# Kernel optimization log

Measured on AMD Instinct MI355X. Metric: run time of the kernel, lower is better.

## Reference

```python
import jax, jax.numpy as jnp
import numpy as np

T, B, DIM, N = 2048, 8, 1024, 64

def setup_inputs() -> dict:
    key = jax.random.key(0)
    ks = jax.random.split(key, 6)
    scale = 1.0 / np.sqrt(DIM)  # xavier-ish for Linear(dim, n_state)
    return {
        "x": jax.random.normal(ks[0], (T, B, DIM), dtype=jnp.float32),
        "S0": jnp.zeros((B, N, N), dtype=jnp.float32),
        "W_k": jax.random.normal(ks[1], (N, DIM), dtype=jnp.float32) * scale,
        "W_v": jax.random.normal(ks[2], (N, DIM), dtype=jnp.float32) * scale,
        "W_q": jax.random.normal(ks[3], (N, DIM), dtype=jnp.float32) * scale,
        "W_alpha": jax.random.normal(ks[4], (N, DIM), dtype=jnp.float32) * scale,
        "b_alpha": jnp.full((N,), 2.0, dtype=jnp.float32),
        "d_g": jnp.full((N,), 0.5, dtype=jnp.float32),
        "b_g": jnp.zeros((N,), dtype=jnp.float32),
    }

def reference(x, S0, W_k, W_v, W_q, W_alpha, b_alpha, d_g, b_g):
    # Precompute all projections: [T, B, N]
    k_all = jnp.einsum('tbd,nd->tbn', x, W_k)
    v_all = jnp.einsum('tbd,nd->tbn', x, W_v)
    q_all = jnp.einsum('tbd,nd->tbn', x, W_q)
    alpha_all = jax.nn.sigmoid(jnp.einsum('tbd,nd->tbn', x, W_alpha) + b_alpha)

    def step(S, inp):
        k, v, q, alpha = inp  # each [B, N]
        retrieved = jnp.einsum('bij,bj->bi', S, k)          # S @ k
        g = jax.nn.sigmoid(d_g * retrieved + b_g)
        v_gated = v * g
        outer_vk = jnp.einsum('bi,bj->bij', v_gated, k)
        S = alpha[..., None] * S + (1.0 - alpha[..., None]) * outer_vk
        out = jnp.einsum('bij,bj->bi', S, q)                # S @ q
        out = out * jax.nn.silu(out)                        # self-gate
        return S, out

    S_final, output = jax.lax.scan(step, S0, (k_all, v_all, q_all, alpha_all))
    return output, S_final
```

## Files before the change

kernel.cpp:

```cpp
#include <hip/hip_runtime.h>

#define TT 2048
#define BB 8
#define DD 1024
#define NN 64
#define C64 64
#define NC2 (TT / C64)

typedef __attribute__((ext_vector_type(8))) short bfrag;
typedef __attribute__((ext_vector_type(4))) float f32x4;
typedef __attribute__((ext_vector_type(8))) unsigned short ushort8;

__device__ __forceinline__ float rcp_(float x) { return __builtin_amdgcn_rcpf(x); }
__device__ __forceinline__ float exp2_(float x) {
#if __has_builtin(__builtin_amdgcn_exp2f)
    return __builtin_amdgcn_exp2f(x);
#else
    return exp2f(x);
#endif
}
__device__ __forceinline__ float sigmoidf_(float x) {
    return rcp_(1.0f + __expf(-x));
}
__device__ __forceinline__ float bcastlane(float x, int l) {
    return __int_as_float(__builtin_amdgcn_readlane(__float_as_int(x), l));
}

__device__ __forceinline__ unsigned short cvt_bf16(float f) {
    unsigned int u = __float_as_uint(f);
    return (unsigned short)((u + 0x7FFF + ((u >> 16) & 1)) >> 16);
}

__device__ __forceinline__ void gll16(const float* g, float* l) {
    __builtin_amdgcn_global_load_lds(
        (const __attribute__((address_space(1))) void*)g,
        (__attribute__((address_space(3))) void*)l, 16, 0, 0);
}

__global__ __launch_bounds__(256) void proj_gemm_kernel(
    const float* __restrict__ x,
    const float* __restrict__ W0, const float* __restrict__ W1,
    const float* __restrict__ W2, const float* __restrict__ W3,
    const float* __restrict__ b_alpha,
    float* __restrict__ O0, float* __restrict__ O1,
    float* __restrict__ O2, float* __restrict__ O3)
{
    const int mat = blockIdx.x;
    const float* __restrict__ W = (mat == 0) ? W0 : (mat == 1) ? W1 : (mat == 2) ? W2 : W3;
    float* __restrict__ C       = (mat == 0) ? O0 : (mat == 1) ? O1 : (mat == 2) ? O2 : O3;

    const int m0   = blockIdx.y * 128;
    const int tid  = threadIdx.x;
    const int lane = tid & 63;
    const int wave = tid >> 6;
    const int ln   = lane & 15;
    const int q8   = (lane >> 4) * 8;

    __shared__ unsigned short As[128][40];
    __shared__ unsigned short Bs[64][40];

    f32x4 acc[2][4] = {};

    const int arow = tid >> 1;
    const int aseg = (tid & 1) * 16;

    float4 pa[4], pb[4];
    {
        const float* ap = &x[(size_t)(m0 + arow) * DD + aseg];
        #pragma unroll
        for (int j = 0; j < 4; j++) pa[j] = *(const float4*)(ap + 4 * j);
        if (tid < 128) {
            const float* bp = &W[(size_t)arow * DD + aseg];
            #pragma unroll
            for (int j = 0; j < 4; j++) pb[j] = *(const float4*)(bp + 4 * j);
        }
    }

    for (int k0 = 0; k0 < DD; k0 += 32) {
        __syncthreads();
        {
            unsigned short t16[16];
            const float* pf = (const float*)pa;
            #pragma unroll
            for (int j = 0; j < 16; j++) t16[j] = cvt_bf16(pf[j]);
            *(ushort8*)&As[arow][aseg]     = *(ushort8*)&t16[0];
            *(ushort8*)&As[arow][aseg + 8] = *(ushort8*)&t16[8];
            if (tid < 128) {
                const float* qf = (const float*)pb;
                #pragma unroll
                for (int j = 0; j < 16; j++) t16[j] = cvt_bf16(qf[j]);
                *(ushort8*)&Bs[arow][aseg]     = *(ushort8*)&t16[0];
                *(ushort8*)&Bs[arow][aseg + 8] = *(ushort8*)&t16[8];
            }
        }
        if (k0 + 32 < DD) {
            const float* ap = &x[(size_t)(m0 + arow) * DD + k0 + 32 + aseg];
            #pragma unroll
            for (int j = 0; j < 4; j++) pa[j] = *(const float4*)(ap + 4 * j);
            if (tid < 128) {
                const float* bp = &W[(size_t)arow * DD + k0 + 32 + aseg];
                #pragma unroll
                for (int j = 0; j < 4; j++) pb[j] = *(const float4*)(bp + 4 * j);
            }
        }
        __syncthreads();

        bfrag af[2], bf[4];
        #pragma unroll
        for (int mt = 0; mt < 2; mt++)
            af[mt] = *(const bfrag*)&As[wave * 32 + mt * 16 + ln][q8];
        #pragma unroll
        for (int nt = 0; nt < 4; nt++)
            bf[nt] = *(const bfrag*)&Bs[nt * 16 + ln][q8];
        #pragma unroll
        for (int mt = 0; mt < 2; mt++)
            #pragma unroll
            for (int nt = 0; nt < 4; nt++)
                acc[mt][nt] = __builtin_amdgcn_mfma_f32_16x16x32_bf16(
                    af[mt], bf[nt], acc[mt][nt], 0, 0, 0);
    }

    #pragma unroll
    for (int nt = 0; nt < 4; nt++) {
        const int col = nt * 16 + ln;
        const float ba = (mat == 3) ? b_alpha[col] : 0.0f;
        #pragma unroll
        for (int mt = 0; mt < 2; mt++) {
            #pragma unroll
            for (int r = 0; r < 4; r++) {
                const int row = m0 + wave * 32 + mt * 16 + (lane >> 4) * 4 + r;
                float v = acc[mt][nt][r];
                if (mat == 3) v = sigmoidf_(v + ba);
                C[(size_t)row * NN + col] = v;
            }
        }
    }
}

__global__ __launch_bounds__(256) void gram_kernel(
    const float* __restrict__ k_all, const float* __restrict__ q_all,
    float* __restrict__ gkq)
{
    const int c  = blockIdx.x;
    const int b  = blockIdx.y;
    const int t0 = c * C64;
    const int tid = threadIdx.x;

    __shared__ __align__(16) float Ks[64][68];
    __shared__ __align__(16) float Qs[64][68];

    {
        const int r = tid >> 2, sg = (tid & 3) * 16;
        const float* kp = &k_all[(size_t)(t0 + r) * (BB * NN) + b * NN + sg];
        const float* qp = &q_all[(size_t)(t0 + r) * (BB * NN) + b * NN + sg];
        #pragma unroll
        for (int j = 0; j < 4; ++j) {
            *(float4*)&Ks[r][sg + 4 * j] = *(const float4*)(kp + 4 * j);
            *(float4*)&Qs[r][sg + 4 * j] = *(const float4*)(qp + 4 * j);
        }
    }
    __syncthreads();

    const int ti = tid >> 4, tj = tid & 15;
    float g[4][4] = {}, kq[4][4] = {};
    #pragma unroll
    for (int c4 = 0; c4 < 16; ++c4) {
        float4 ka[4], kb[4], qb[4];
        #pragma unroll
        for (int r = 0; r < 4; ++r) {
            ka[r] = *(const float4*)&Ks[4 * ti + r][c4 * 4];
            kb[r] = *(const float4*)&Ks[4 * tj + r][c4 * 4];
            qb[r] = *(const float4*)&Qs[4 * tj + r][c4 * 4];
        }
        #pragma unroll
        for (int r = 0; r < 4; ++r)
            #pragma unroll
            for (int q = 0; q < 4; ++q) {
                g[r][q]  = fmaf(ka[r].x, kb[q].x, g[r][q]);
                g[r][q]  = fmaf(ka[r].y, kb[q].y, g[r][q]);
                g[r][q]  = fmaf(ka[r].z, kb[q].z, g[r][q]);
                g[r][q]  = fmaf(ka[r].w, kb[q].w, g[r][q]);
                kq[r][q] = fmaf(ka[r].x, qb[q].x, kq[r][q]);
                kq[r][q] = fmaf(ka[r].y, qb[q].y, kq[r][q]);
                kq[r][q] = fmaf(ka[r].z, qb[q].z, kq[r][q]);
                kq[r][q] = fmaf(ka[r].w, qb[q].w, kq[r][q]);
            }
    }

    float* base = gkq + (size_t)(b * NC2 + c) * 64 * 128;
    #pragma unroll
    for (int r = 0; r < 4; ++r) {
        const int s = 4 * ti + r;
        #pragma unroll
        for (int q = 0; q < 4; ++q) {
            const int t = 4 * tj + q;
            float2 gv; gv.x = g[r][q]; gv.y = kq[r][q];
            *(float2*)&base[s * 128 + 2 * t] = gv;
        }
    }
}

__global__ __launch_bounds__(256) void scan_kernel(
    const float* __restrict__ gkq,
    const float* __restrict__ k_all, const float* __restrict__ q_all,
    const float* __restrict__ a_all, const float* __restrict__ v_all,
    const float* __restrict__ S0,
    const float* __restrict__ d_g, const float* __restrict__ b_g,
    float* __restrict__ out, float* __restrict__ S_final)
{
    const int b    = blockIdx.x;
    const int rg   = blockIdx.y;
    const int tid  = threadIdx.x;
    const int lane = tid & 63;
    const int wave = tid >> 6;
    const int row  = rg * 4 + wave;

    __shared__ __align__(16) float gk[2][64 * 128];
    __shared__ __align__(16) float Kl[2][64 * 64];
    __shared__ __align__(16) float Ql[2][64 * 64];
    __shared__ __align__(16) float unif[4][256];
    __shared__ __align__(16) float sbuf[4][64];

    float S = S0[((size_t)b * NN + row) * NN + lane];
    const float L2E  = 1.4426950408889634f;
    const float ndg2 = -d_g[row] * L2E;
    const float nbg2 = -b_g[row] * L2E;

    const float* gkq_b = gkq + (size_t)b * NC2 * 64 * 128;

    const int s_loc = lane >> 4;
    const int gr    = lane & 15;

    auto stage = [&](int c, int db) {
        const float* src = gkq_b + (size_t)c * 64 * 128;
        #pragma unroll
        for (int j = 0; j < 8; ++j) {
            const int off = (wave * 16 + 2 * j) * 128;
            gll16(src + off + lane * 4, &gk[db][off]);
        }
        #pragma unroll
        for (int j = 0; j < 4; ++j) {
            const int r0 = wave * 16 + 4 * j;
            const int s  = r0 + s_loc;
            const int gg = gr ^ (s & 15);
            const size_t goff = ((size_t)(c * C64 + s) * BB + b) * NN + gg * 4;
            gll16(k_all + goff, &Kl[db][r0 * 64]);
            gll16(q_all + goff, &Ql[db][r0 * 64]);
        }
    };

    float a_nx, v_nx;
    auto aw_load = [&](int c) {
        const size_t goff = ((size_t)(c * C64 + lane) * BB + b) * NN + row;
        a_nx = a_all[goff];
        v_nx = v_all[goff];
    };

    stage(0, 0);
    aw_load(0);

    for (int c = 0; c < NC2; ++c) {
        const int db = c & 1;
        const float ac = a_nx;
        const float wc = (1.0f - a_nx) * v_nx;
        __syncthreads();
        if (c + 1 < NC2) { aw_load(c + 1); stage(c + 1, db ^ 1); }

        float P = ac;
        #pragma unroll
        for (int off = 1; off < 64; off <<= 1) {
            float v = __shfl_up(P, off, 64);
            if (lane >= off) P *= v;
        }
        float Pm = __shfl_up(P, 1, 64);
        if (lane == 0) Pm = 1.0f;
        const float u = wc * rcp_(P);

        sbuf[wave][lane] = S;
        const float* Kb = &Kl[db][0];
        const float* Qb = &Ql[db][0];
        float4 ha = {0.f, 0.f, 0.f, 0.f};
        float4 hb = {0.f, 0.f, 0.f, 0.f};
        #pragma unroll
        for (int g4 = 0; g4 < 16; ++g4) {
            const int idx = lane * 64 + ((g4 ^ (lane & 15)) << 2);
            float4 kv = *(const float4*)&Kb[idx];
            float4 qv = *(const float4*)&Qb[idx];
            float4 sv = *(const float4*)&sbuf[wave][g4 << 2];
            ha.x = fmaf(kv.x, sv.x, ha.x); ha.y = fmaf(kv.y, sv.y, ha.y);
            ha.z = fmaf(kv.z, sv.z, ha.z); ha.w = fmaf(kv.w, sv.w, ha.w);
            hb.x = fmaf(qv.x, sv.x, hb.x); hb.y = fmaf(qv.y, sv.y, hb.y);
            hb.z = fmaf(qv.z, sv.z, hb.z); hb.w = fmaf(qv.w, sv.w, hb.w);
        }
        const float h  = (ha.x + ha.y) + (ha.z + ha.w);
        const float hq = (hb.x + hb.y) + (hb.z + hb.w);
        const float e1 = ndg2 * Pm;
        const float e0 = fmaf(e1, h, nbg2);
        {
            float4 uv; uv.x = e1; uv.y = e0; uv.z = u; uv.w = 0.0f;
            *(float4*)&unif[wave][lane * 4] = uv;
        }

        float A = 0.f, Bacc = 0.f, Bl = 0.f, Sa = 0.f;
        const float* gkb = &gk[db][0];
        float2 gk_c = *(const float2*)&gkb[lane * 2];
        float  k_c  = Kb[lane];
        float4 u_c  = *(const float4*)&unif[wave][0];

        for (int s8 = 0; s8 < 64; s8 += 8) {
            #pragma unroll
            for (int k = 0; k < 8; ++k) {
                const int s  = s8 + k;
                const int sn = (s + 1) & 63;
                float2 gk_n = *(const float2*)&gkb[sn * 128 + lane * 2];
                float  k_n  = Kb[sn * 64 + (lane ^ ((sn & 15) << 2))];
                float4 u_n  = *(const float4*)&unif[wave][sn * 4];

                const float Ab = bcastlane(A, s);
                const float ch = u_c.z *
                    rcp_(1.0f + exp2_(fmaf(u_c.x, Ab, u_c.y)));
                A    = fmaf(ch, gk_c.x, A);
                Bacc = fmaf(ch, gk_c.y, Bacc);
                Sa   = fmaf(ch, k_c,    Sa);
                Bl   = (lane == s) ? Bacc : Bl;
                gk_c = gk_n; k_c = k_n; u_c = u_n;
            }
        }

        const float o = P * (hq + Bl);
        const float y = o * o * rcp_(1.0f + exp2_(-o * L2E));
        out[((size_t)(c * C64 + lane) * BB + b) * NN + row] = y;
        const float Pl = bcastlane(P, 63);
        S = Pl * (S + Sa);
    }

    S_final[((size_t)b * NN + row) * NN + lane] = S;
}

extern "C" void kernel_launch(void* const* d_in, const int* in_sizes, int n_in,
                              void* d_out, int out_size, void* d_ws, size_t ws_size,
                              hipStream_t stream) {
    const float* x       = (const float*)d_in[0];
    const float* S0      = (const float*)d_in[1];
    const float* W_k     = (const float*)d_in[2];
    const float* W_v     = (const float*)d_in[3];
    const float* W_q     = (const float*)d_in[4];
    const float* W_alpha = (const float*)d_in[5];
    const float* b_alpha = (const float*)d_in[6];
    const float* d_g     = (const float*)d_in[7];
    const float* b_g     = (const float*)d_in[8];
    float* out = (float*)d_out;

    const size_t arr = (size_t)TT * BB * NN;
    float* ws    = (float*)d_ws;
    float* k_all = ws;
    float* v_all = ws + arr;
    float* q_all = ws + 2 * arr;
    float* a_all = ws + 3 * arr;
    float* gkq   = ws + 4 * arr;

    proj_gemm_kernel<<<dim3(4, TT * BB / 128), 256, 0, stream>>>(
        x, W_k, W_v, W_q, W_alpha, b_alpha, k_all, v_all, q_all, a_all);

    gram_kernel<<<dim3(NC2, BB), 256, 0, stream>>>(k_all, q_all, gkq);

    scan_kernel<<<dim3(BB, 16), 256, 0, stream>>>(
        gkq, k_all, q_all, a_all, v_all, S0, d_g, b_g, out, out + arr);
}
```

Measured before the change: 317.6 us.

## Transpose gram layout, register-resident scan loop, DPP prefix product

The gram/KQ chunk matrices are now stored transposed with an XOR swizzle, so each lane can load its full column of G and KQ into registers before the sequential inner loop. The 64-step recurrence then reads only registers and uses one readlane per step, instead of issuing LDS loads and a uniform-buffer lookup every step. The Sa accumulation moves to a separate pass that broadcasts the stored per-step coefficients. The shuffle-based prefix product is replaced by a DPP row-shift/broadcast sequence, and Pm is computed as P/ac. Holding 128 floats in registers per lane raises register pressure, and launch bounds are set to one block per SM to allow it.

```diff
diff --git a/kernel.cpp b/kernel.cpp
--- a/kernel.cpp
+++ b/kernel.cpp
@@ -24,6 +24,22 @@
 }
 __device__ __forceinline__ float bcastlane(float x, int l) {
     return __int_as_float(__builtin_amdgcn_readlane(__float_as_int(x), l));
+}
+
+template <int CTRL, int RM>
+__device__ __forceinline__ float dpp_mul1(float x) {
+    int v = __builtin_amdgcn_update_dpp(
+        0x3f800000, __float_as_int(x), CTRL, RM, 0xF, false);
+    return x * __int_as_float(v);
+}
+__device__ __forceinline__ float prefix_mul64(float x) {
+    x = dpp_mul1<0x111, 0xF>(x);
+    x = dpp_mul1<0x112, 0xF>(x);
+    x = dpp_mul1<0x114, 0xF>(x);
+    x = dpp_mul1<0x118, 0xF>(x);
+    x = dpp_mul1<0x142, 0xA>(x);
+    x = dpp_mul1<0x143, 0xC>(x);
+    return x;
 }
 
 __device__ __forceinline__ unsigned short cvt_bf16(float f) {
@@ -190,17 +206,17 @@
     float* base = gkq + (size_t)(b * NC2 + c) * 64 * 128;
     #pragma unroll
     for (int r = 0; r < 4; ++r) {
-        const int s = 4 * ti + r;
         #pragma unroll
         for (int q = 0; q < 4; ++q) {
-            const int t = 4 * tj + q;
-            float2 gv; gv.x = g[r][q]; gv.y = kq[r][q];
-            *(float2*)&base[s * 128 + 2 * t] = gv;
-        }
-    }
-}
-
-__global__ __launch_bounds__(256) void scan_kernel(
+            const int t   = 4 * tj + q;
+            const int pos = ((ti ^ (t & 15)) << 2) + r;
+            base[t * 128 + pos]      = g[r][q];
+            base[t * 128 + 64 + pos] = kq[r][q];
+        }
+    }
+}
+
+__global__ __launch_bounds__(256, 1) void scan_kernel(
     const float* __restrict__ gkq,
     const float* __restrict__ k_all, const float* __restrict__ q_all,
     const float* __restrict__ a_all, const float* __restrict__ v_all,
@@ -215,10 +231,9 @@
     const int wave = tid >> 6;
     const int row  = rg * 4 + wave;
 
-    __shared__ __align__(16) float gk[2][64 * 128];
+    __shared__ __align__(16) float gT[2][64 * 128];
     __shared__ __align__(16) float Kl[2][64 * 64];
     __shared__ __align__(16) float Ql[2][64 * 64];
-    __shared__ __align__(16) float unif[4][256];
     __shared__ __align__(16) float sbuf[4][64];
 
     float S = S0[((size_t)b * NN + row) * NN + lane];
@@ -236,7 +251,7 @@
         #pragma unroll
         for (int j = 0; j < 8; ++j) {
             const int off = (wave * 16 + 2 * j) * 128;
-            gll16(src + off + lane * 4, &gk[db][off]);
+            gll16(src + off + lane * 4, &gT[db][off]);
         }
         #pragma unroll
         for (int j = 0; j < 4; ++j) {
@@ -266,15 +281,9 @@
         __syncthreads();
         if (c + 1 < NC2) { aw_load(c + 1); stage(c + 1, db ^ 1); }
 
-        float P = ac;
-        #pragma unroll
-        for (int off = 1; off < 64; off <<= 1) {
-            float v = __shfl_up(P, off, 64);
-            if (lane >= off) P *= v;
-        }
-        float Pm = __shfl_up(P, 1, 64);
-        if (lane == 0) Pm = 1.0f;
-        const float u = wc * rcp_(P);
+        const float P  = prefix_mul64(ac);
+        const float Pm = P / ac;
+        const float u  = wc * rcp_(P);
 
         sbuf[wave][lane] = S;
         const float* Kb = &Kl[db][0];
@@ -283,7 +292,7 @@
         float4 hb = {0.f, 0.f, 0.f, 0.f};
         #pragma unroll
         for (int g4 = 0; g4 < 16; ++g4) {
-            const int idx = lane * 64 + ((g4 ^ (lane & 15)) << 2);
+            const int idx = lane * 64 + ((g4 ^ gr) << 2);
             float4 kv = *(const float4*)&Kb[idx];
             float4 qv = *(const float4*)&Qb[idx];
             float4 sv = *(const float4*)&sbuf[wave][g4 << 2];
@@ -296,35 +305,39 @@
         const float hq = (hb.x + hb.y) + (hb.z + hb.w);
         const float e1 = ndg2 * Pm;
         const float e0 = fmaf(e1, h, nbg2);
+
+        float Ga[64], Qa[64];
         {
-            float4 uv; uv.x = e1; uv.y = e0; uv.z = u; uv.w = 0.0f;
-            *(float4*)&unif[wave][lane * 4] = uv;
-        }
-
-        float A = 0.f, Bacc = 0.f, Bl = 0.f, Sa = 0.f;
-        const float* gkb = &gk[db][0];
-        float2 gk_c = *(const float2*)&gkb[lane * 2];
-        float  k_c  = Kb[lane];
-        float4 u_c  = *(const float4*)&unif[wave][0];
-
-        for (int s8 = 0; s8 < 64; s8 += 8) {
-            #pragma unroll
-            for (int k = 0; k < 8; ++k) {
-                const int s  = s8 + k;
-                const int sn = (s + 1) & 63;
-                float2 gk_n = *(const float2*)&gkb[sn * 128 + lane * 2];
-                float  k_n  = Kb[sn * 64 + (lane ^ ((sn & 15) << 2))];
-                float4 u_n  = *(const float4*)&unif[wave][sn * 4];
-
-                const float Ab = bcastlane(A, s);
-                const float ch = u_c.z *
-                    rcp_(1.0f + exp2_(fmaf(u_c.x, Ab, u_c.y)));
-                A    = fmaf(ch, gk_c.x, A);
-                Bacc = fmaf(ch, gk_c.y, Bacc);
-                Sa   = fmaf(ch, k_c,    Sa);
-                Bl   = (lane == s) ? Bacc : Bl;
-                gk_c = gk_n; k_c = k_n; u_c = u_n;
-            }
+            const float* gt = &gT[db][0];
+            #pragma unroll
+            for (int j = 0; j < 16; ++j) {
+                const int addr = lane * 128 + ((j ^ gr) << 2);
+                const float4 gv = *(const float4*)&gt[addr];
+                const float4 qv = *(const float4*)&gt[addr + 64];
+                Ga[4 * j + 0] = gv.x; Ga[4 * j + 1] = gv.y;
+                Ga[4 * j + 2] = gv.z; Ga[4 * j + 3] = gv.w;
+                Qa[4 * j + 0] = qv.x; Qa[4 * j + 1] = qv.y;
+                Qa[4 * j + 2] = qv.z; Qa[4 * j + 3] = qv.w;
+            }
+        }
+
+        float A = 0.f, Bacc = 0.f, Bl = 0.f, chl = 0.f;
+        #pragma unroll
+        for (int s = 0; s < 64; ++s) {
+            const float sg  = rcp_(1.0f + exp2_(fmaf(e1, A, e0)));
+            const float s2  = sg * u;
+            const float chs = bcastlane(s2, s);
+            A    = fmaf(chs, Ga[s], A);
+            Bacc = fmaf(chs, Qa[s], Bacc);
+            if (lane == s) { Bl = Bacc; chl = chs; }
+        }
+
+        float Sa = 0.f;
+        #pragma unroll
+        for (int s = 0; s < 64; ++s) {
+            const float chs = bcastlane(chl, s);
+            const float kv  = Kb[s * 64 + (((lane >> 2) ^ (s & 15)) << 2) + (lane & 3)];
+            Sa = fmaf(chs, kv, Sa);
         }
 
         const float o = P * (hq + Bl);
```

Measured after the change: 326.5 us. 1.03x slower.
